# Performance work log

Measured on AMD Instinct MI355X. Metric: run time of the kernel, lower is better.

## Reference

```python
import jax, jax.numpy as jnp
import numpy as np

N = 100000   # nodes
E = 1600000  # edges
F_IN = 128
H = 128      # hidden_channels
G = 1000     # graphs in batch
EPS = 1e-5


def setup_inputs() -> dict:
    key = jax.random.key(0)
    ks = jax.random.split(key, 20)
    x = jax.random.normal(ks[0], (N, F_IN), dtype=jnp.float32)
    edge_index = jax.random.randint(ks[1], (2, E), 0, N, dtype=jnp.int64)
    batch = jnp.sort(jax.random.randint(ks[2], (N,), 0, G, dtype=jnp.int64))
    s = 0.05
    inp = {
        "x": x,
        "edge_index": edge_index,
        "batch": batch,
        "W1": jax.random.normal(ks[3], (F_IN, H), dtype=jnp.float32) * s,
        "b1": jnp.zeros((H,), jnp.float32),
        "g1": jnp.ones((H,), jnp.float32),
        "be1": jnp.zeros((H,), jnp.float32),
        "W2": jax.random.normal(ks[4], (H, H), dtype=jnp.float32) * s,
        "b2": jnp.zeros((H,), jnp.float32),
        "g2": jnp.ones((H,), jnp.float32),
        "be2": jnp.zeros((H,), jnp.float32),
        "W3": jax.random.normal(ks[5], (H, H), dtype=jnp.float32) * s,
        "b3": jnp.zeros((H,), jnp.float32),
        "g3": jnp.ones((H,), jnp.float32),
        "be3": jnp.zeros((H,), jnp.float32),
        "Wl": jax.random.normal(ks[6], (H, 1), dtype=jnp.float32) * s,
        "bl": jnp.zeros((1,), jnp.float32),
    }
    return inp


def _gcn_conv(x, W, b, src, dst, dinv):
    # PyG GCNConv: h = x W; out[d] = sum_e dinv[src]*dinv[dst]*h[src]; out += b
    h = x @ W
    coef = (dinv[src] * dinv[dst])[:, None]
    msg = h[src] * coef                       # [E+N, H] gather + scale
    out = jax.ops.segment_sum(msg, dst, num_segments=N)
    return out + b


def _bn_relu(x, g, be):
    # BatchNorm1d training mode: batch stats, biased variance
    m = jnp.mean(x, axis=0)
    v = jnp.var(x, axis=0)
    xn = (x - m) * jax.lax.rsqrt(v + EPS)
    return jax.nn.relu(xn * g + be)


def reference(x, edge_index, batch, W1, b1, g1, be1, W2, b2, g2, be2,
              W3, b3, g3, be3, Wl, bl):
    loop = jnp.arange(N, dtype=edge_index.dtype)
    src = jnp.concatenate([edge_index[0], loop])  # self-loops appended
    dst = jnp.concatenate([edge_index[1], loop])
    deg = jax.ops.segment_sum(jnp.ones_like(dst, dtype=x.dtype), dst,
                              num_segments=N)
    dinv = jax.lax.rsqrt(deg)                     # deg >= 1 (self-loops)

    h = _bn_relu(_gcn_conv(x, W1, b1, src, dst, dinv), g1, be1)
    h = _bn_relu(_gcn_conv(h, W2, b2, src, dst, dinv), g2, be2)
    h = _bn_relu(_gcn_conv(h, W3, b3, src, dst, dinv), g3, be3)

    # global_mean_pool over graph ids
    sums = jax.ops.segment_sum(h, batch, num_segments=G)
    cnt = jax.ops.segment_sum(jnp.ones((N,), h.dtype), batch, num_segments=G)
    pooled = sums / jnp.maximum(cnt, 1.0)[:, None]

    return pooled @ Wl + bl
```

## Files before the change

### kernel.cpp

```cpp
#include <hip/hip_runtime.h>
#include <hip/hip_bf16.h>

#define Nn 100000
#define Ee 1600000
#define Hh 128
#define Gg 1000
#define EPSb 1e-5f

#define AGG_BLOCKS 2048
#define NWAVES (AGG_BLOCKS * 4)
#define GEMM_BLOCKS 391

#define BKT 196
#define BSTRIDE 12288
#define FILL_CHUNK 4096
#define FILL_BLOCKS 391

typedef unsigned int uint;
typedef short short8 __attribute__((ext_vector_type(8)));
typedef float floatx4 __attribute__((ext_vector_type(4)));

static __device__ __forceinline__ uint bf16rne(float f) {
    uint u = __float_as_uint(f);
    return (u + 0x7fffu + ((u >> 16) & 1u)) >> 16;
}
static __device__ __forceinline__ float bflo(uint u) { return __uint_as_float(u << 16); }
static __device__ __forceinline__ float bfhi(uint u) { return __uint_as_float(u & 0xffff0000u); }


__global__ __launch_bounds__(256) void k_bucket(
    const int* __restrict__ src, const int* __restrict__ dst,
    int* __restrict__ deg, int* __restrict__ bcnt, uint* __restrict__ stage) {
    __shared__ int cnt[BKT];
    __shared__ int base[BKT];
    int t = threadIdx.x;
    if (t < BKT) cnt[t] = 0;
    __syncthreads();
    int e0 = blockIdx.x * FILL_CHUNK;
    int slot[16], bkt[16];
#pragma unroll
    for (int j = 0; j < 16; ++j) {
        int i = e0 + j * 256 + t;
        if (i < Ee) {
            int dd = dst[i];
            atomicAdd(&deg[dd], 1);
            int b = dd >> 9;
            bkt[j] = b;
            slot[j] = atomicAdd(&cnt[b], 1);
        } else bkt[j] = -1;
    }
    __syncthreads();
    if (t < BKT) base[t] = atomicAdd(&bcnt[t], cnt[t]);
    __syncthreads();
#pragma unroll
    for (int j = 0; j < 16; ++j) {
        if (bkt[j] >= 0) {
            int i = e0 + j * 256 + t;
            int b = bkt[j];
            int p = base[b] + slot[j];
            if (p < BSTRIDE)
                stage[(size_t)b * BSTRIDE + p] =
                    (uint)src[i] | (((uint)dst[i] & 511u) << 17);
        }
    }
}

__global__ __launch_bounds__(256) void k_scan3b(
    const int* __restrict__ deg, const int* __restrict__ bcnt,
    int* __restrict__ offs, float* __restrict__ dinv) {
    __shared__ int ls[256];
    __shared__ int bs[256];
    int t = threadIdx.x;
    int b = blockIdx.x;
    bs[t] = (t < BKT) ? bcnt[t] : 0;
    int base = (b << 9) + t * 2;
    int d0 = (base     < Nn) ? deg[base]     : 0;
    int d1 = (base + 1 < Nn) ? deg[base + 1] : 0;
    int s = d0 + d1;
    ls[t] = s;
    __syncthreads();
    for (int off = 1; off < 256; off <<= 1) {
        int u0 = (t >= off) ? bs[t - off] : 0;
        int u1 = (t >= off) ? ls[t - off] : 0;
        __syncthreads();
        bs[t] += u0;
        ls[t] += u1;
        __syncthreads();
    }
    int bucketBase = (b == 0) ? 0 : bs[b - 1];
    int run = bucketBase + ls[t] - s;
    if (base < Nn) {
        offs[base] = run;
        dinv[base] = rsqrtf((float)(d0 + 1));
    }
    run += d0;
    if (base + 1 < Nn) {
        offs[base + 1] = run;
        dinv[base + 1] = rsqrtf((float)(d1 + 1));
    }
    if (b == 0 && t == 0) offs[Nn] = Ee;
}

__global__ __launch_bounds__(256) void k_scatter(
    const int* __restrict__ bcnt, const uint* __restrict__ stage,
    const int* __restrict__ offs, int* __restrict__ adj) {
    __shared__ int lcur[512];
    int b = blockIdx.x;
    int t = threadIdx.x;
    lcur[t] = 0; lcur[t + 256] = 0;
    __syncthreads();
    int n = bcnt[b];
    if (n > BSTRIDE) n = BSTRIDE;
    int dbase = b << 9;
    const uint* sp = stage + (size_t)b * BSTRIDE;
    for (int i = t; i < n; i += 256) {
        uint e = sp[i];
        int s = (int)(e & 0x1FFFFu);
        int dl = (int)(e >> 17);
        int pos = offs[dbase + dl] + atomicAdd(&lcur[dl], 1);
        adj[pos] = s;
    }
}


__global__ void k_wconv3(const float* __restrict__ W1, const float* __restrict__ W2,
                         const float* __restrict__ W3, uint* __restrict__ Wt) {
    int idx = blockIdx.x * blockDim.x + threadIdx.x;
    if (idx >= 3 * 8192) return;
    const float* W = (idx < 8192) ? W1 : ((idx < 16384) ? W2 : W3);
    int k = idx & 8191;
    int n = k >> 6, ku = k & 63;
    uint lo = bf16rne(W[(size_t)(2 * ku) * 128 + n]);
    uint hi = bf16rne(W[(size_t)(2 * ku + 1) * 128 + n]);
    Wt[(size_t)(idx >> 13) * 8192 + n * 64 + ku] = lo | (hi << 16);
}


__global__ __launch_bounds__(256, 2) void k_gemm(
    const float* __restrict__ inf, const uint* __restrict__ inb,
    const uint* __restrict__ Wtp, const float* __restrict__ dinv,
    const float* __restrict__ cs, const float* __restrict__ gg,
    const float* __restrict__ be,
    uint* __restrict__ outb, int mode) {
    __shared__ uint XT[128][64];
    __shared__ uint WT[128][64];
    __shared__ float scsh[256];
    int t = threadIdx.x;
    int r = t >> 1, half = t & 1;

    if (mode && t < 128) {
        float s = cs[t], q = cs[128 + t];
        float m = s * (1.0f / Nn);
        float var = q * (1.0f / Nn) - m * m;
        float istd = rsqrtf(var + EPSb);
        float sc = istd * gg[t];
        scsh[t] = sc;
        scsh[128 + t] = fmaf(-m, sc, be[t]);
    }
    {
        const uint* sp = Wtp + (size_t)r * 64 + half * 32;
#pragma unroll
        for (int q = 0; q < 8; ++q) {
            uint4 v = *(const uint4*)(sp + q * 4);
            int g = half * 8 + q;
            *(uint4*)&WT[r][(g ^ (r & 7)) << 2] = v;
        }
    }

    float4 xf[16];
    uint4  xb[8];

    int rb0 = blockIdx.x * 128;
    {
        int grc = rb0 + r;
        if (grc >= Nn) grc = Nn - 1;
        if (mode == 0) {
            const float* sp = inf + (size_t)grc * 128 + half * 64;
#pragma unroll
            for (int q = 0; q < 8; ++q) {
                xf[2 * q]     = *(const float4*)(sp + q * 8);
                xf[2 * q + 1] = *(const float4*)(sp + q * 8 + 4);
            }
        } else {
            const uint* sp = inb + (size_t)grc * 64 + half * 32;
#pragma unroll
            for (int q = 0; q < 8; ++q) xb[q] = *(const uint4*)(sp + q * 4);
        }
    }
    __syncthreads();

#pragma unroll
    for (int q = 0; q < 8; ++q) {
        uint4 o;
        if (mode == 0) {
            float4 v0 = xf[2 * q], v1 = xf[2 * q + 1];
            o.x = bf16rne(v0.x) | (bf16rne(v0.y) << 16);
            o.y = bf16rne(v0.z) | (bf16rne(v0.w) << 16);
            o.z = bf16rne(v1.x) | (bf16rne(v1.y) << 16);
            o.w = bf16rne(v1.z) | (bf16rne(v1.w) << 16);
        } else {
            uint4 v = xb[q];
            int fb = half * 64 + q * 8;
            float av[8] = {bflo(v.x), bfhi(v.x), bflo(v.y), bfhi(v.y),
                           bflo(v.z), bfhi(v.z), bflo(v.w), bfhi(v.w)};
            uint oo[4];
#pragma unroll
            for (int k2 = 0; k2 < 4; ++k2) {
                float lo = fmaxf(fmaf(av[2 * k2], scsh[fb + 2 * k2],
                                      scsh[128 + fb + 2 * k2]), 0.f);
                float hi = fmaxf(fmaf(av[2 * k2 + 1], scsh[fb + 2 * k2 + 1],
                                      scsh[128 + fb + 2 * k2 + 1]), 0.f);
                oo[k2] = bf16rne(lo) | (bf16rne(hi) << 16);
            }
            o = make_uint4(oo[0], oo[1], oo[2], oo[3]);
        }
        int g = half * 8 + q;
        *(uint4*)&XT[r][(g ^ (r & 7)) << 2] = o;
    }
    __syncthreads();

    int l = t & 63, w = t >> 6;
    int nb = (w >> 1) * 64;
    int fb2 = (w & 1) * 64;
    int lr = l & 15, lk = l >> 4;
    floatx4 zero = {0.f, 0.f, 0.f, 0.f};

    int rb1 = (blockIdx.x + GEMM_BLOCKS) * 128;
    {
        int grc = rb1 + r;
        if (grc >= Nn) grc = Nn - 1;
        if (mode == 0) {
            const float* sp = inf + (size_t)grc * 128 + half * 64;
#pragma unroll
            for (int q = 0; q < 8; ++q) {
                xf[2 * q]     = *(const float4*)(sp + q * 8);
                xf[2 * q + 1] = *(const float4*)(sp + q * 8 + 4);
            }
        } else {
            const uint* sp = inb + (size_t)grc * 64 + half * 32;
#pragma unroll
            for (int q = 0; q < 8; ++q) xb[q] = *(const uint4*)(sp + q * 4);
        }
    }

    {
        floatx4 acc[4][4];
#pragma unroll
        for (int mi = 0; mi < 4; ++mi)
#pragma unroll
            for (int ni = 0; ni < 4; ++ni) acc[mi][ni] = zero;
#pragma unroll
        for (int kc = 0; kc < 4; ++kc) {
            short8 xfr[4], wfr[4];
            int g = kc * 4 + lk;
#pragma unroll
            for (int mi = 0; mi < 4; ++mi) {
                int rr = nb + mi * 16 + lr;
                xfr[mi] = *(const short8*)&XT[rr][(g ^ (rr & 7)) << 2];
            }
#pragma unroll
            for (int ni = 0; ni < 4; ++ni) {
                int rr = fb2 + ni * 16 + lr;
                wfr[ni] = *(const short8*)&WT[rr][(g ^ (rr & 7)) << 2];
            }
#pragma unroll
            for (int mi = 0; mi < 4; ++mi)
#pragma unroll
                for (int ni = 0; ni < 4; ++ni)
                    acc[mi][ni] = __builtin_amdgcn_mfma_f32_16x16x32_bf16(
                        wfr[ni], xfr[mi], acc[mi][ni], 0, 0, 0);
        }
#pragma unroll
        for (int mi = 0; mi < 4; ++mi) {
            int node = rb0 + nb + mi * 16 + lr;
            if (node < Nn) {
                float dv = dinv[node];
                uint* op = outb + (size_t)node * 64;
#pragma unroll
                for (int ni = 0; ni < 4; ++ni) {
                    int fo = fb2 + ni * 16 + lk * 4;
                    uint2 o;
                    o.x = bf16rne(acc[mi][ni][0] * dv) | (bf16rne(acc[mi][ni][1] * dv) << 16);
                    o.y = bf16rne(acc[mi][ni][2] * dv) | (bf16rne(acc[mi][ni][3] * dv) << 16);
                    *(uint2*)(op + (fo >> 1)) = o;
                }
            }
        }
    }
    __syncthreads();

#pragma unroll
    for (int q = 0; q < 8; ++q) {
        uint4 o;
        if (mode == 0) {
            float4 v0 = xf[2 * q], v1 = xf[2 * q + 1];
            o.x = bf16rne(v0.x) | (bf16rne(v0.y) << 16);
            o.y = bf16rne(v0.z) | (bf16rne(v0.w) << 16);
            o.z = bf16rne(v1.x) | (bf16rne(v1.y) << 16);
            o.w = bf16rne(v1.z) | (bf16rne(v1.w) << 16);
        } else {
            uint4 v = xb[q];
            int fb = half * 64 + q * 8;
            float av[8] = {bflo(v.x), bfhi(v.x), bflo(v.y), bfhi(v.y),
                           bflo(v.z), bfhi(v.z), bflo(v.w), bfhi(v.w)};
            uint oo[4];
#pragma unroll
            for (int k2 = 0; k2 < 4; ++k2) {
                float lo = fmaxf(fmaf(av[2 * k2], scsh[fb + 2 * k2],
                                      scsh[128 + fb + 2 * k2]), 0.f);
                float hi = fmaxf(fmaf(av[2 * k2 + 1], scsh[fb + 2 * k2 + 1],
                                      scsh[128 + fb + 2 * k2 + 1]), 0.f);
                oo[k2] = bf16rne(lo) | (bf16rne(hi) << 16);
            }
            o = make_uint4(oo[0], oo[1], oo[2], oo[3]);
        }
        int g = half * 8 + q;
        *(uint4*)&XT[r][(g ^ (r & 7)) << 2] = o;
    }
    __syncthreads();

    {
        floatx4 acc[4][4];
#pragma unroll
        for (int mi = 0; mi < 4; ++mi)
#pragma unroll
            for (int ni = 0; ni < 4; ++ni) acc[mi][ni] = zero;
#pragma unroll
        for (int kc = 0; kc < 4; ++kc) {
            short8 xfr[4], wfr[4];
            int g = kc * 4 + lk;
#pragma unroll
            for (int mi = 0; mi < 4; ++mi) {
                int rr = nb + mi * 16 + lr;
                xfr[mi] = *(const short8*)&XT[rr][(g ^ (rr & 7)) << 2];
            }
#pragma unroll
            for (int ni = 0; ni < 4; ++ni) {
                int rr = fb2 + ni * 16 + lr;
                wfr[ni] = *(const short8*)&WT[rr][(g ^ (rr & 7)) << 2];
            }
#pragma unroll
            for (int mi = 0; mi < 4; ++mi)
#pragma unroll
                for (int ni = 0; ni < 4; ++ni)
                    acc[mi][ni] = __builtin_amdgcn_mfma_f32_16x16x32_bf16(
                        wfr[ni], xfr[mi], acc[mi][ni], 0, 0, 0);
        }
#pragma unroll
        for (int mi = 0; mi < 4; ++mi) {
            int node = rb1 + nb + mi * 16 + lr;
            if (node < Nn) {
                float dv = dinv[node];
                uint* op = outb + (size_t)node * 64;
#pragma unroll
                for (int ni = 0; ni < 4; ++ni) {
                    int fo = fb2 + ni * 16 + lk * 4;
                    uint2 o;
                    o.x = bf16rne(acc[mi][ni][0] * dv) | (bf16rne(acc[mi][ni][1] * dv) << 16);
                    o.y = bf16rne(acc[mi][ni][2] * dv) | (bf16rne(acc[mi][ni][3] * dv) << 16);
                    *(uint2*)(op + (fo >> 1)) = o;
                }
            }
        }
    }
}


__global__ __launch_bounds__(256) void k_agg(
    const uint* __restrict__ h32, const int* __restrict__ offs,
    const int* __restrict__ adj, const float* __restrict__ dinv,
    const float* __restrict__ bias, uint* __restrict__ agg,
    float* __restrict__ colsum) {
    __shared__ float ls[256];
    int tid = threadIdx.x;
    ls[tid] = 0.f;
    __syncthreads();
    int lane = tid & 63;
    int gw = blockIdx.x * 4 + (tid >> 6);
    int nw = NWAVES;
    int c0 = lane * 2;
    float b0 = bias[c0], b1 = bias[c0 + 1];
    float ps0 = 0.f, pq0 = 0.f, ps1 = 0.f, pq1 = 0.f;
    for (int d = gw; d < Nn; d += nw) {
        int beg = offs[d], end = offs[d + 1];
        float dvd = dinv[d];
        uint hself = h32[(size_t)d * 64 + lane];
        float a0 = bflo(hself), a1 = bfhi(hself);
        int i = beg;
        for (; i + 8 <= end; i += 8) {
            int e[8];
#pragma unroll
            for (int j = 0; j < 8; ++j) e[j] = adj[i + j];
            uint hv[8];
#pragma unroll
            for (int j = 0; j < 8; ++j)
                hv[j] = h32[(size_t)e[j] * 64 + lane];
#pragma unroll
            for (int j = 0; j < 8; ++j) {
                a0 += bflo(hv[j]);
                a1 += bfhi(hv[j]);
            }
        }
        for (; i < end; ++i) {
            uint hv = h32[(size_t)adj[i] * 64 + lane];
            a0 += bflo(hv);
            a1 += bfhi(hv);
        }
        a0 = fmaf(a0, dvd, b0);
        a1 = fmaf(a1, dvd, b1);
        agg[(size_t)d * 64 + lane] = bf16rne(a0) | (bf16rne(a1) << 16);
        ps0 += a0; pq0 += a0 * a0;
        ps1 += a1; pq1 += a1 * a1;
    }
    atomicAdd(&ls[c0], ps0);
    atomicAdd(&ls[c0 + 1], ps1);
    atomicAdd(&ls[128 + c0], pq0);
    atomicAdd(&ls[128 + c0 + 1], pq1);
    __syncthreads();
    atomicAdd(&colsum[tid], ls[tid]);
}


__global__ __launch_bounds__(256) void k_pool(
    const uint* __restrict__ agg, const int* __restrict__ batch,
    const float* __restrict__ cs, const float* __restrict__ gg,
    const float* __restrict__ be,
    const float* __restrict__ Wl, const float* __restrict__ bl,
    float* __restrict__ out) {
    __shared__ float scsh[256];
    int tid = threadIdx.x;
    if (tid < 128) {
        float s = cs[tid], q = cs[128 + tid];
        float m = s * (1.0f / Nn);
        float var = q * (1.0f / Nn) - m * m;
        float istd = rsqrtf(var + EPSb);
        float sc = istd * gg[tid];
        scsh[tid] = sc;
        scsh[128 + tid] = fmaf(-m, sc, be[tid]);
    }
    __syncthreads();
    int lane = tid & 63;
    int g = (blockIdx.x * blockDim.x + tid) >> 6;
    if (g >= Gg) return;
    int lo = 0, hi = Nn;
    while (lo < hi) { int mid = (lo + hi) >> 1; if (batch[mid] < g) lo = mid + 1; else hi = mid; }
    int beg = lo;
    hi = Nn;
    while (lo < hi) { int mid = (lo + hi) >> 1; if (batch[mid] < g + 1) lo = mid + 1; else hi = mid; }
    int end = lo;
    int c0 = lane * 2;
    float sc0 = scsh[c0], sh0 = scsh[128 + c0];
    float sc1 = scsh[c0 + 1], sh1 = scsh[128 + c0 + 1];
    float s0 = 0.f, s1 = 0.f;
    for (int n = beg; n < end; ++n) {
        uint v = agg[(size_t)n * 64 + lane];
        s0 += fmaxf(fmaf(bflo(v), sc0, sh0), 0.f);
        s1 += fmaxf(fmaf(bfhi(v), sc1, sh1), 0.f);
    }
    float inv = 1.0f / fmaxf((float)(end - beg), 1.0f);
    float part = (s0 * inv) * Wl[c0] + (s1 * inv) * Wl[c0 + 1];
#pragma unroll
    for (int off = 32; off; off >>= 1) part += __shfl_down(part, off);
    if (lane == 0) out[g] = part + bl[0];
}


extern "C" void kernel_launch(void* const* d_in, const int* in_sizes, int n_in,
                              void* d_out, int out_size, void* d_ws, size_t ws_size,
                              hipStream_t stream) {
    const float* x   = (const float*)d_in[0];
    const int*   ei  = (const int*)d_in[1];
    const int*   src = ei;
    const int*   dst = ei + Ee;
    const int*   bat = (const int*)d_in[2];
    const float* W1 = (const float*)d_in[3];
    const float* b1 = (const float*)d_in[4];
    const float* g1 = (const float*)d_in[5];
    const float* be1 = (const float*)d_in[6];
    const float* W2 = (const float*)d_in[7];
    const float* b2 = (const float*)d_in[8];
    const float* g2 = (const float*)d_in[9];
    const float* be2 = (const float*)d_in[10];
    const float* W3 = (const float*)d_in[11];
    const float* b3 = (const float*)d_in[12];
    const float* g3 = (const float*)d_in[13];
    const float* be3 = (const float*)d_in[14];
    const float* Wl = (const float*)d_in[15];
    const float* bl = (const float*)d_in[16];
    float* out = (float*)d_out;

    char* w = (char*)d_ws;
    auto alloc = [&](size_t bytes) {
        void* p = (void*)w;
        w += (bytes + 255) & ~(size_t)255;
        return p;
    };
    int*   deg    = (int*)alloc((size_t)Nn * 4);
    int*   bcnt   = (int*)alloc(BKT * 4);
    float* colsum = (float*)alloc(768 * 4);
    size_t zspan  = (size_t)((char*)(colsum + 768) - (char*)deg);
    int*   offs   = (int*)alloc((size_t)(Nn + 1) * 4);
    float* dinv   = (float*)alloc((size_t)Nn * 4);
    uint*  Wt     = (uint*)alloc((size_t)3 * 8192 * 4);
    uint*  stage  = (uint*)alloc((size_t)BKT * BSTRIDE * 4);
    int*   adj    = (int*)alloc((size_t)Ee * 4);
    uint*  tmp    = (uint*)alloc((size_t)Nn * 64 * 4);
    uint*  agg    = (uint*)alloc((size_t)Nn * 64 * 4);

    float* csA = colsum;
    float* csB = colsum + 256;
    float* csC = colsum + 512;

    hipMemsetAsync(deg, 0, zspan, stream);
    k_bucket<<<FILL_BLOCKS, 256, 0, stream>>>(src, dst, deg, bcnt, stage);
    k_scan3b<<<BKT, 256, 0, stream>>>(deg, bcnt, offs, dinv);
    k_scatter<<<BKT, 256, 0, stream>>>(bcnt, stage, offs, adj);
    k_wconv3<<<96, 256, 0, stream>>>(W1, W2, W3, Wt);
    k_gemm<<<GEMM_BLOCKS, 256, 0, stream>>>(x, (const uint*)0, Wt, dinv,
                                            (const float*)0, (const float*)0,
                                            (const float*)0, tmp, 0);
    k_agg<<<AGG_BLOCKS, 256, 0, stream>>>(tmp, offs, adj, dinv, b1, agg, csA);
    k_gemm<<<GEMM_BLOCKS, 256, 0, stream>>>((const float*)0, agg, Wt + 8192, dinv,
                                            csA, g1, be1, tmp, 1);
    k_agg<<<AGG_BLOCKS, 256, 0, stream>>>(tmp, offs, adj, dinv, b2, agg, csB);
    k_gemm<<<GEMM_BLOCKS, 256, 0, stream>>>((const float*)0, agg, Wt + 16384, dinv,
                                            csB, g2, be2, tmp, 1);
    k_agg<<<AGG_BLOCKS, 256, 0, stream>>>(tmp, offs, adj, dinv, b3, agg, csC);
    k_pool<<<(Gg * 64 + 255) / 256, 256, 0, stream>>>(agg, bat, csC, g3, be3,
                                                      Wl, bl, out);
}
```

Measured before the change: 545.9 us.

## Fuse scan and scatter kernels; make GEMM load operands directly without LDS

Merges the degree scan and the CSR scatter into one kernel that keeps per-bucket offsets in shared memory, which removes one launch and the global reads of offs. Rewrites the bf16 MFMA GEMM so each wave loads its X and W fragments straight from global memory into registers. This drops the LDS staging, the barriers and the two-tile software pipeline, and doubles the block count to one 128-row tile per block. The risk is more redundant global and L2 traffic for W and X fragments, plus less latency hiding without the prefetch of the second tile.

```diff
diff --git a/kernel.cpp b/kernel.cpp
--- a/kernel.cpp
+++ b/kernel.cpp
@@ -9,7 +9,7 @@
 
 #define AGG_BLOCKS 2048
 #define NWAVES (AGG_BLOCKS * 4)
-#define GEMM_BLOCKS 391
+#define GEMM_BLOCKS 782
 
 #define BKT 196
 #define BSTRIDE 12288
@@ -65,14 +65,19 @@
     }
 }
 
-__global__ __launch_bounds__(256) void k_scan3b(
+__global__ __launch_bounds__(256) void k_prep(
     const int* __restrict__ deg, const int* __restrict__ bcnt,
-    int* __restrict__ offs, float* __restrict__ dinv) {
+    const uint* __restrict__ stage,
+    int* __restrict__ offs, float* __restrict__ dinv, int* __restrict__ adj) {
     __shared__ int ls[256];
     __shared__ int bs[256];
+    __shared__ int loffs[512];
+    __shared__ int lcur[512];
     int t = threadIdx.x;
     int b = blockIdx.x;
+    lcur[t] = 0; lcur[t + 256] = 0;
     bs[t] = (t < BKT) ? bcnt[t] : 0;
+    int nEdges = bcnt[b];
     int base = (b << 9) + t * 2;
     int d0 = (base     < Nn) ? deg[base]     : 0;
     int d1 = (base + 1 < Nn) ? deg[base + 1] : 0;
@@ -89,36 +94,27 @@
     }
     int bucketBase = (b == 0) ? 0 : bs[b - 1];
     int run = bucketBase + ls[t] - s;
+    loffs[t * 2] = run;
     if (base < Nn) {
         offs[base] = run;
         dinv[base] = rsqrtf((float)(d0 + 1));
     }
     run += d0;
+    loffs[t * 2 + 1] = run;
     if (base + 1 < Nn) {
         offs[base + 1] = run;
         dinv[base + 1] = rsqrtf((float)(d1 + 1));
     }
     if (b == 0 && t == 0) offs[Nn] = Ee;
-}
-
-__global__ __launch_bounds__(256) void k_scatter(
-    const int* __restrict__ bcnt, const uint* __restrict__ stage,
-    const int* __restrict__ offs, int* __restrict__ adj) {
-    __shared__ int lcur[512];
-    int b = blockIdx.x;
-    int t = threadIdx.x;
-    lcur[t] = 0; lcur[t + 256] = 0;
-    __syncthreads();
-    int n = bcnt[b];
-    if (n > BSTRIDE) n = BSTRIDE;
-    int dbase = b << 9;
+    __syncthreads();
+    int n = nEdges > BSTRIDE ? BSTRIDE : nEdges;
     const uint* sp = stage + (size_t)b * BSTRIDE;
     for (int i = t; i < n; i += 256) {
         uint e = sp[i];
-        int s = (int)(e & 0x1FFFFu);
+        int s2 = (int)(e & 0x1FFFFu);
         int dl = (int)(e >> 17);
-        int pos = offs[dbase + dl] + atomicAdd(&lcur[dl], 1);
-        adj[pos] = s;
+        int pos = loffs[dl] + atomicAdd(&lcur[dl], 1);
+        adj[pos] = s2;
     }
 }
 
@@ -136,230 +132,116 @@
 }
 
 
-__global__ __launch_bounds__(256, 2) void k_gemm(
+__global__ __launch_bounds__(256) void k_gemm(
     const float* __restrict__ inf, const uint* __restrict__ inb,
     const uint* __restrict__ Wtp, const float* __restrict__ dinv,
     const float* __restrict__ cs, const float* __restrict__ gg,
     const float* __restrict__ be,
     uint* __restrict__ outb, int mode) {
-    __shared__ uint XT[128][64];
-    __shared__ uint WT[128][64];
-    __shared__ float scsh[256];
+    __shared__ __attribute__((aligned(16))) float scsh[256];
     int t = threadIdx.x;
-    int r = t >> 1, half = t & 1;
-
-    if (mode && t < 128) {
-        float s = cs[t], q = cs[128 + t];
-        float m = s * (1.0f / Nn);
-        float var = q * (1.0f / Nn) - m * m;
-        float istd = rsqrtf(var + EPSb);
-        float sc = istd * gg[t];
-        scsh[t] = sc;
-        scsh[128 + t] = fmaf(-m, sc, be[t]);
-    }
-    {
-        const uint* sp = Wtp + (size_t)r * 64 + half * 32;
-#pragma unroll
-        for (int q = 0; q < 8; ++q) {
-            uint4 v = *(const uint4*)(sp + q * 4);
-            int g = half * 8 + q;
-            *(uint4*)&WT[r][(g ^ (r & 7)) << 2] = v;
-        }
-    }
-
-    float4 xf[16];
-    uint4  xb[8];
-
-    int rb0 = blockIdx.x * 128;
-    {
-        int grc = rb0 + r;
-        if (grc >= Nn) grc = Nn - 1;
-        if (mode == 0) {
-            const float* sp = inf + (size_t)grc * 128 + half * 64;
-#pragma unroll
-            for (int q = 0; q < 8; ++q) {
-                xf[2 * q]     = *(const float4*)(sp + q * 8);
-                xf[2 * q + 1] = *(const float4*)(sp + q * 8 + 4);
-            }
-        } else {
-            const uint* sp = inb + (size_t)grc * 64 + half * 32;
-#pragma unroll
-            for (int q = 0; q < 8; ++q) xb[q] = *(const uint4*)(sp + q * 4);
-        }
-    }
-    __syncthreads();
-
-#pragma unroll
-    for (int q = 0; q < 8; ++q) {
-        uint4 o;
-        if (mode == 0) {
-            float4 v0 = xf[2 * q], v1 = xf[2 * q + 1];
-            o.x = bf16rne(v0.x) | (bf16rne(v0.y) << 16);
-            o.y = bf16rne(v0.z) | (bf16rne(v0.w) << 16);
-            o.z = bf16rne(v1.x) | (bf16rne(v1.y) << 16);
-            o.w = bf16rne(v1.z) | (bf16rne(v1.w) << 16);
-        } else {
-            uint4 v = xb[q];
-            int fb = half * 64 + q * 8;
-            float av[8] = {bflo(v.x), bfhi(v.x), bflo(v.y), bfhi(v.y),
-                           bflo(v.z), bfhi(v.z), bflo(v.w), bfhi(v.w)};
-            uint oo[4];
-#pragma unroll
-            for (int k2 = 0; k2 < 4; ++k2) {
-                float lo = fmaxf(fmaf(av[2 * k2], scsh[fb + 2 * k2],
-                                      scsh[128 + fb + 2 * k2]), 0.f);
-                float hi = fmaxf(fmaf(av[2 * k2 + 1], scsh[fb + 2 * k2 + 1],
-                                      scsh[128 + fb + 2 * k2 + 1]), 0.f);
-                oo[k2] = bf16rne(lo) | (bf16rne(hi) << 16);
-            }
-            o = make_uint4(oo[0], oo[1], oo[2], oo[3]);
-        }
-        int g = half * 8 + q;
-        *(uint4*)&XT[r][(g ^ (r & 7)) << 2] = o;
-    }
-    __syncthreads();
+    if (mode) {
+        if (t < 128) {
+            float s = cs[t], q = cs[128 + t];
+            float m = s * (1.0f / Nn);
+            float var = q * (1.0f / Nn) - m * m;
+            float istd = rsqrtf(var + EPSb);
+            float sc = istd * gg[t];
+            scsh[t] = sc;
+            scsh[128 + t] = fmaf(-m, sc, be[t]);
+        }
+        __syncthreads();
+    }
 
     int l = t & 63, w = t >> 6;
+    int rowBase = blockIdx.x * 128;
     int nb = (w >> 1) * 64;
     int fb2 = (w & 1) * 64;
     int lr = l & 15, lk = l >> 4;
+
+    int nd[4];
+#pragma unroll
+    for (int mi = 0; mi < 4; ++mi) {
+        int node = rowBase + nb + mi * 16 + lr;
+        nd[mi] = node < Nn ? node : Nn - 1;
+    }
+
     floatx4 zero = {0.f, 0.f, 0.f, 0.f};
-
-    int rb1 = (blockIdx.x + GEMM_BLOCKS) * 128;
-    {
-        int grc = rb1 + r;
-        if (grc >= Nn) grc = Nn - 1;
+    floatx4 acc[4][4];
+#pragma unroll
+    for (int mi = 0; mi < 4; ++mi)
+#pragma unroll
+        for (int ni = 0; ni < 4; ++ni) acc[mi][ni] = zero;
+
+#pragma unroll
+    for (int kc = 0; kc < 4; ++kc) {
+        int g = kc * 4 + lk;
+        short8 xf[4], wf[4];
         if (mode == 0) {
-            const float* sp = inf + (size_t)grc * 128 + half * 64;
-#pragma unroll
-            for (int q = 0; q < 8; ++q) {
-                xf[2 * q]     = *(const float4*)(sp + q * 8);
-                xf[2 * q + 1] = *(const float4*)(sp + q * 8 + 4);
+#pragma unroll
+            for (int mi = 0; mi < 4; ++mi) {
+                const float* sp = inf + (size_t)nd[mi] * 128 + g * 8;
+                float4 v0 = *(const float4*)sp;
+                float4 v1 = *(const float4*)(sp + 4);
+                uint4 o;
+                o.x = bf16rne(v0.x) | (bf16rne(v0.y) << 16);
+                o.y = bf16rne(v0.z) | (bf16rne(v0.w) << 16);
+                o.z = bf16rne(v1.x) | (bf16rne(v1.y) << 16);
+                o.w = bf16rne(v1.z) | (bf16rne(v1.w) << 16);
+                union { uint4 u; short8 s; } cvt;
+                cvt.u = o;
+                xf[mi] = cvt.s;
             }
         } else {
-            const uint* sp = inb + (size_t)grc * 64 + half * 32;
-#pragma unroll
-            for (int q = 0; q < 8; ++q) xb[q] = *(const uint4*)(sp + q * 4);
-        }
-    }
-
-    {
-        floatx4 acc[4][4];
+            float4 s0 = *(const float4*)(scsh + g * 8);
+            float4 s1 = *(const float4*)(scsh + g * 8 + 4);
+            float4 h0 = *(const float4*)(scsh + 128 + g * 8);
+            float4 h1 = *(const float4*)(scsh + 128 + g * 8 + 4);
+#pragma unroll
+            for (int mi = 0; mi < 4; ++mi) {
+                uint4 v = *(const uint4*)(inb + (size_t)nd[mi] * 64 + g * 4);
+                float a0 = fmaxf(fmaf(bflo(v.x), s0.x, h0.x), 0.f);
+                float a1 = fmaxf(fmaf(bfhi(v.x), s0.y, h0.y), 0.f);
+                float a2 = fmaxf(fmaf(bflo(v.y), s0.z, h0.z), 0.f);
+                float a3 = fmaxf(fmaf(bfhi(v.y), s0.w, h0.w), 0.f);
+                float a4 = fmaxf(fmaf(bflo(v.z), s1.x, h1.x), 0.f);
+                float a5 = fmaxf(fmaf(bfhi(v.z), s1.y, h1.y), 0.f);
+                float a6 = fmaxf(fmaf(bflo(v.w), s1.z, h1.z), 0.f);
+                float a7 = fmaxf(fmaf(bfhi(v.w), s1.w, h1.w), 0.f);
+                uint4 o;
+                o.x = bf16rne(a0) | (bf16rne(a1) << 16);
+                o.y = bf16rne(a2) | (bf16rne(a3) << 16);
+                o.z = bf16rne(a4) | (bf16rne(a5) << 16);
+                o.w = bf16rne(a6) | (bf16rne(a7) << 16);
+                union { uint4 u; short8 s; } cvt;
+                cvt.u = o;
+                xf[mi] = cvt.s;
+            }
+        }
+#pragma unroll
+        for (int ni = 0; ni < 4; ++ni)
+            wf[ni] = *(const short8*)(Wtp + (size_t)(fb2 + ni * 16 + lr) * 64 + g * 4);
 #pragma unroll
         for (int mi = 0; mi < 4; ++mi)
 #pragma unroll
-            for (int ni = 0; ni < 4; ++ni) acc[mi][ni] = zero;
-#pragma unroll
-        for (int kc = 0; kc < 4; ++kc) {
-            short8 xfr[4], wfr[4];
-            int g = kc * 4 + lk;
-#pragma unroll
-            for (int mi = 0; mi < 4; ++mi) {
-                int rr = nb + mi * 16 + lr;
-                xfr[mi] = *(const short8*)&XT[rr][(g ^ (rr & 7)) << 2];
-            }
+            for (int ni = 0; ni < 4; ++ni)
+                acc[mi][ni] = __builtin_amdgcn_mfma_f32_16x16x32_bf16(
+                    wf[ni], xf[mi], acc[mi][ni], 0, 0, 0);
+    }
+
+#pragma unroll
+    for (int mi = 0; mi < 4; ++mi) {
+        int node = rowBase + nb + mi * 16 + lr;
+        if (node < Nn) {
+            float dv = dinv[node];
+            uint* op = outb + (size_t)node * 64;
 #pragma unroll
             for (int ni = 0; ni < 4; ++ni) {
-                int rr = fb2 + ni * 16 + lr;
-                wfr[ni] = *(const short8*)&WT[rr][(g ^ (rr & 7)) << 2];
-            }
-#pragma unroll
-            for (int mi = 0; mi < 4; ++mi)
-#pragma unroll
-                for (int ni = 0; ni < 4; ++ni)
-                    acc[mi][ni] = __builtin_amdgcn_mfma_f32_16x16x32_bf16(
-                        wfr[ni], xfr[mi], acc[mi][ni], 0, 0, 0);
-        }
-#pragma unroll
-        for (int mi = 0; mi < 4; ++mi) {
-            int node = rb0 + nb + mi * 16 + lr;
-            if (node < Nn) {
-                float dv = dinv[node];
-                uint* op = outb + (size_t)node * 64;
-#pragma unroll
-                for (int ni = 0; ni < 4; ++ni) {
-                    int fo = fb2 + ni * 16 + lk * 4;
-                    uint2 o;
-                    o.x = bf16rne(acc[mi][ni][0] * dv) | (bf16rne(acc[mi][ni][1] * dv) << 16);
-                    o.y = bf16rne(acc[mi][ni][2] * dv) | (bf16rne(acc[mi][ni][3] * dv) << 16);
-                    *(uint2*)(op + (fo >> 1)) = o;
-                }
-            }
-        }
-    }
-    __syncthreads();
-
-#pragma unroll
-    for (int q = 0; q < 8; ++q) {
-        uint4 o;
-        if (mode == 0) {
-            float4 v0 = xf[2 * q], v1 = xf[2 * q + 1];
-            o.x = bf16rne(v0.x) | (bf16rne(v0.y) << 16);
-            o.y = bf16rne(v0.z) | (bf16rne(v0.w) << 16);
-            o.z = bf16rne(v1.x) | (bf16rne(v1.y) << 16);
-            o.w = bf16rne(v1.z) | (bf16rne(v1.w) << 16);
-        } else {
-            uint4 v = xb[q];
-            int fb = half * 64 + q * 8;
-            float av[8] = {bflo(v.x), bfhi(v.x), bflo(v.y), bfhi(v.y),
-                           bflo(v.z), bfhi(v.z), bflo(v.w), bfhi(v.w)};
-            uint oo[4];
-#pragma unroll
-            for (int k2 = 0; k2 < 4; ++k2) {
-                float lo = fmaxf(fmaf(av[2 * k2], scsh[fb + 2 * k2],
-                                      scsh[128 + fb + 2 * k2]), 0.f);
-                float hi = fmaxf(fmaf(av[2 * k2 + 1], scsh[fb + 2 * k2 + 1],
-                                      scsh[128 + fb + 2 * k2 + 1]), 0.f);
-                oo[k2] = bf16rne(lo) | (bf16rne(hi) << 16);
-            }
-            o = make_uint4(oo[0], oo[1], oo[2], oo[3]);
-        }
-        int g = half * 8 + q;
-        *(uint4*)&XT[r][(g ^ (r & 7)) << 2] = o;
-    }
-    __syncthreads();
-
-    {
-        floatx4 acc[4][4];
-#pragma unroll
-        for (int mi = 0; mi < 4; ++mi)
-#pragma unroll
-            for (int ni = 0; ni < 4; ++ni) acc[mi][ni] = zero;
-#pragma unroll
-        for (int kc = 0; kc < 4; ++kc) {
-            short8 xfr[4], wfr[4];
-            int g = kc * 4 + lk;
-#pragma unroll
-            for (int mi = 0; mi < 4; ++mi) {
-                int rr = nb + mi * 16 + lr;
-                xfr[mi] = *(const short8*)&XT[rr][(g ^ (rr & 7)) << 2];
-            }
-#pragma unroll
-            for (int ni = 0; ni < 4; ++ni) {
-                int rr = fb2 + ni * 16 + lr;
-                wfr[ni] = *(const short8*)&WT[rr][(g ^ (rr & 7)) << 2];
-            }
-#pragma unroll
-            for (int mi = 0; mi < 4; ++mi)
-#pragma unroll
-                for (int ni = 0; ni < 4; ++ni)
-                    acc[mi][ni] = __builtin_amdgcn_mfma_f32_16x16x32_bf16(
-                        wfr[ni], xfr[mi], acc[mi][ni], 0, 0, 0);
-        }
-#pragma unroll
-        for (int mi = 0; mi < 4; ++mi) {
-            int node = rb1 + nb + mi * 16 + lr;
-            if (node < Nn) {
-                float dv = dinv[node];
-                uint* op = outb + (size_t)node * 64;
-#pragma unroll
-                for (int ni = 0; ni < 4; ++ni) {
-                    int fo = fb2 + ni * 16 + lk * 4;
-                    uint2 o;
-                    o.x = bf16rne(acc[mi][ni][0] * dv) | (bf16rne(acc[mi][ni][1] * dv) << 16);
-                    o.y = bf16rne(acc[mi][ni][2] * dv) | (bf16rne(acc[mi][ni][3] * dv) << 16);
-                    *(uint2*)(op + (fo >> 1)) = o;
-                }
+                int fo = fb2 + ni * 16 + lk * 4;
+                uint2 o;
+                o.x = bf16rne(acc[mi][ni][0] * dv) | (bf16rne(acc[mi][ni][1] * dv) << 16);
+                o.y = bf16rne(acc[mi][ni][2] * dv) | (bf16rne(acc[mi][ni][3] * dv) << 16);
+                *(uint2*)(op + (fo >> 1)) = o;
             }
         }
     }
@@ -513,8 +395,7 @@
 
     hipMemsetAsync(deg, 0, zspan, stream);
     k_bucket<<<FILL_BLOCKS, 256, 0, stream>>>(src, dst, deg, bcnt, stage);
-    k_scan3b<<<BKT, 256, 0, stream>>>(deg, bcnt, offs, dinv);
-    k_scatter<<<BKT, 256, 0, stream>>>(bcnt, stage, offs, adj);
+    k_prep<<<BKT, 256, 0, stream>>>(deg, bcnt, stage, offs, dinv, adj);
     k_wconv3<<<96, 256, 0, stream>>>(W1, W2, W3, Wt);
     k_gemm<<<GEMM_BLOCKS, 256, 0, stream>>>(x, (const uint*)0, Wt, dinv,
                                             (const float*)0, (const float*)0,
```

Measured after the change: 563.5 us. 3.2% more time.
